# Optimization experiments

Hardware: AMD Instinct MI355X
Metric: run time of the kernel (lower is better)

The kernel has to match this reference:

```python
import jax, jax.numpy as jnp
import numpy as np

# PtConv dims from SegSmall: pl=64 channels, n_centers=16 kernel elements, dim=3
B, N, K = 4, 16384, 16          # batch, points, neighbors
C_IN, C_OUT, KS, DIM = 64, 64, 16, 3


def setup_inputs() -> dict:
    key = jax.random.key(0)
    ks = jax.random.split(key, 10)
    features = jax.random.normal(ks[0], (B, N, C_IN), dtype=jnp.float32)
    input_pts = jax.random.uniform(ks[1], (B, N, DIM), dtype=jnp.float32)
    output_pts = input_pts  # same-resolution conv: queries == input points
    indices = jax.random.randint(ks[2], (B, N, K), 0, N)  # precomputed KNN indices
    # weight init as in PtConv
    bound = float(np.sqrt(3.0) * np.sqrt(2.0 / (C_IN + C_OUT)))
    weight = jax.random.uniform(ks[3], (C_IN, KS, C_OUT), jnp.float32, -bound, bound)
    bias = jnp.zeros((C_OUT,), jnp.float32)
    centers = jax.random.uniform(ks[4], (DIM, KS), jnp.float32, -1.0, 1.0)
    # position-MLP params: Linear(dim*KS -> 2*KS), Linear(2*KS -> KS), Linear(KS -> KS)
    def lin(k, fan_in, fan_out):
        lim = 1.0 / np.sqrt(fan_in)
        kw, kb = jax.random.split(k)
        W = jax.random.uniform(kw, (fan_in, fan_out), jnp.float32, -lim, lim)
        b = jax.random.uniform(kb, (fan_out,), jnp.float32, -lim, lim)
        return W, b
    w1, b1 = lin(ks[5], DIM * KS, 2 * KS)
    w2, b2 = lin(ks[6], 2 * KS, KS)
    w3, b3 = lin(ks[7], KS, KS)
    return {"features": features, "input_pts": input_pts, "output_pts": output_pts,
            "weight": weight, "bias": bias, "centers": centers,
            "w1": w1, "b1": b1, "w2": w2, "b2": b2, "w3": w3, "b3": b3,
            "indices": indices}


def reference(features, input_pts, output_pts, weight, bias, centers,
              w1, b1, w2, b2, w3, b3, indices):
    # per-batch gather of neighbor features and coordinates
    gather = jax.vmap(lambda a, idx: a[idx])
    feat_g = gather(features, indices)          # [B, M, K, C_in]
    pts_g = gather(input_pts, indices)          # [B, M, K, 3]
    pts = pts_g - output_pts[:, :, None, :]      # nn_center=True
    # distances to kernel centers: [B,M,K,3,1] - [3,KS] -> [B,M,K,3,KS] -> [B,M,K,3*KS]
    d = (pts[..., None] - centers).reshape(pts.shape[0], pts.shape[1], pts.shape[2], -1)
    d = jax.nn.relu(d @ w1 + b1)
    d = jax.nn.relu(d @ w2 + b2)
    d = jax.nn.relu(d @ w3 + b3)                 # [B, M, K, KS]
    # weighted neighbor aggregation: bmm(features^T, dists)
    agg = jnp.einsum('bmkc,bmkj->bmcj', feat_g, d)   # [B, M, C_in, KS]
    out = jnp.einsum('bmcj,cjo->bmo', agg, weight)   # flatten (C_in,KS) matches weight.view(-1,out)
    out = out / feat_g.shape[2]                      # divide by K (fs[2])
    out = out + bias
    return out
```

## Files before the change

kernel.cpp:

```cpp
#include <hip/hip_runtime.h>

#define NPTS 16384
#define KN   16
#define CIN  64
#define COUT 64
#define KSIZ 16
#define PTS  16

typedef _Float16 h4v    __attribute__((ext_vector_type(4)));
typedef _Float16 h8v    __attribute__((ext_vector_type(8)));
typedef __fp16   fp16x2 __attribute__((ext_vector_type(2)));
typedef float    f32x4  __attribute__((ext_vector_type(4)));

union H2U { fp16x2 h; unsigned u; };
union H4U { h4v v; fp16x2 p[2]; };
union H8U { h8v v; uint4 u4; };

__global__ void prep_kernel(const float* __restrict__ weight,
                            const float* __restrict__ w1,
                            const float* __restrict__ b1,
                            const float* __restrict__ centers,
                            unsigned* __restrict__ wsp,
                            uint4* __restrict__ wf) {
    const int b = blockIdx.x;
    const int tid = threadIdx.x;
    if (b == 128) {
        __shared__ float tmp[4][32];
        if (tid < 32) {
            int n = tid;
            float s0 = 0.f, s1 = 0.f, s2 = 0.f, bf = b1[n];
            for (int s = 0; s < KSIZ; ++s) {
                float a0 = w1[(0*KSIZ + s)*32 + n];
                float a1 = w1[(1*KSIZ + s)*32 + n];
                float a2 = w1[(2*KSIZ + s)*32 + n];
                s0 += a0; s1 += a1; s2 += a2;
                bf -= centers[0*KSIZ+s]*a0 + centers[1*KSIZ+s]*a1 + centers[2*KSIZ+s]*a2;
            }
            tmp[0][n] = s0; tmp[1][n] = s1; tmp[2][n] = s2; tmp[3][n] = bf;
        }
        __syncthreads();
        if (tid < 64) {
            const int row = tid >> 4, q = tid & 15;
            union { _Float16 h[2]; unsigned u; } pk;
            pk.h[0] = (_Float16)tmp[row][2*q];
            pk.h[1] = (_Float16)tmp[row][2*q+1];
            wsp[row*16 + q] = pk.u;
        }
        return;
    }
    const int kk = b >> 2, nt = b & 3;
    const int l  = tid, li = l & 15, g = l >> 4;
    unsigned short u[8];
    #pragma unroll
    for (int e = 0; e < 8; ++e) {
        int s = kk*32 + g*8 + e;
        int j = s >> 6;
        int c = s & 63;
        union { _Float16 h; unsigned short s16; } cv;
        cv.h = (_Float16)(weight[(c*16 + j)*64 + nt*16 + li] * 0.0625f);
        u[e] = cv.s16;
    }
    uint4 v;
    v.x = u[0] | ((unsigned)u[1] << 16);
    v.y = u[2] | ((unsigned)u[3] << 16);
    v.z = u[4] | ((unsigned)u[5] << 16);
    v.w = u[6] | ((unsigned)u[7] << 16);
    wf[(kk*4 + nt)*64 + l] = v;
}

__global__ __launch_bounds__(256, 4)
void ptconv_kernel(const float* __restrict__ features,
                   const float* __restrict__ input_pts,
                   const float* __restrict__ output_pts,
                   const float* __restrict__ bias,
                   const float* __restrict__ w2,
                   const float* __restrict__ b2,
                   const float* __restrict__ w3,
                   const float* __restrict__ b3,
                   const int*   __restrict__ indices,
                   const unsigned* __restrict__ folded,
                   const uint4* __restrict__ wf,
                   float* __restrict__ out) {
    __shared__ __align__(16) char smem[34048];
    char* s_agg = smem;
    int*  s_idx = (int*)(smem + 33024);

    const int t    = threadIdx.x;
    const int l    = t & 63;
    const int wave = t >> 6;
    const int li   = l & 15;
    const int g    = l >> 4;
    const int m0   = blockIdx.x * PTS;
    const int bbk  = m0 >> 14;

    const int p1 = t >> 4, k1 = t & 15;
    const int nn = (m0 + p1) & (NPTS-1);
    const int idxv = indices[(bbk*NPTS + nn)*KN + k1];
    s_idx[p1*16 + k1] = idxv;
    const float* ip = input_pts  + (size_t)(bbk*NPTS + idxv)*3;
    const float* op = output_pts + (size_t)(bbk*NPTS + nn)*3;
    const float r0 = ip[0]-op[0], r1 = ip[1]-op[1], r2 = ip[2]-op[2];

    h8v w2f; h4v w3f;
    #pragma unroll
    for (int e = 0; e < 8; ++e) w2f[e] = (_Float16)w2[(8*g+e)*16 + li];
    #pragma unroll
    for (int e = 0; e < 4; ++e) w3f[e] = (_Float16)w3[(4*g+e)*16 + li];
    const f32x4 b2v4  = *(const f32x4*)(b2 + 4*g);
    const float b3v   = b3[li];
    const float biasO = bias[wave*16 + li];

    {
        const __fp16 r0h = (__fp16)r0, r1h = (__fp16)r1, r2h = (__fp16)r2;
        fp16x2 r0p = {r0h, r0h}, r1p = {r1h, r1h}, r2p = {r2h, r2h};
        const fp16x2 zz = {(__fp16)0.f, (__fp16)0.f};
        unsigned o16[16];
        #pragma unroll
        for (int q = 0; q < 16; ++q) {
            H2U a, u0, u1, u2;
            a.u  = folded[48+q];
            u0.u = folded[q];
            u1.u = folded[16+q];
            u2.u = folded[32+q];
            fp16x2 acc = r0p*u0.h + a.h;
            acc = r1p*u1.h + acc;
            acc = r2p*u2.h + acc;
            acc = __builtin_elementwise_max(acc, zz);
            H2U o; o.h = acc; o16[q] = o.u;
        }
        uint4* dst = (uint4*)(smem + wave*8256 + l*80);
        dst[0] = make_uint4(o16[0],  o16[1],  o16[2],  o16[3]);
        dst[1] = make_uint4(o16[4],  o16[5],  o16[6],  o16[7]);
        dst[2] = make_uint4(o16[8],  o16[9],  o16[10], o16[11]);
        dst[3] = make_uint4(o16[12], o16[13], o16[14], o16[15]);
    }

    const float* fb = features + (size_t)bbk*NPTS*CIN;
    f32x4 rv[4][4];
    #pragma unroll
    for (int pp = 0; pp < 4; ++pp) {
        const int p2 = wave*4 + pp;
        const int4 id4 = *(const int4*)(s_idx + p2*16 + 4*g);
        rv[pp][0] = *(const f32x4*)(fb + (size_t)id4.x*CIN + 4*li);
        rv[pp][1] = *(const f32x4*)(fb + (size_t)id4.y*CIN + 4*li);
        rv[pp][2] = *(const f32x4*)(fb + (size_t)id4.z*CIN + 4*li);
        rv[pp][3] = *(const f32x4*)(fb + (size_t)id4.w*CIN + 4*li);
    }

    h4v dreg[4];
    #pragma unroll
    for (int pp = 0; pp < 4; ++pp) {
        h8v B2 = *(const h8v*)(smem + wave*8256 + (pp*16 + li)*80 + g*16);
        f32x4 acc2 = b2v4;
        acc2 = __builtin_amdgcn_mfma_f32_16x16x32_f16(w2f, B2, acc2, 0, 0, 0);
        H4U A3;
        A3.p[0] = __builtin_amdgcn_cvt_pkrtz(fmaxf(acc2[0],0.f), fmaxf(acc2[1],0.f));
        A3.p[1] = __builtin_amdgcn_cvt_pkrtz(fmaxf(acc2[2],0.f), fmaxf(acc2[3],0.f));
        f32x4 acc3 = {b3v, b3v, b3v, b3v};
        acc3 = __builtin_amdgcn_mfma_f32_16x16x16f16(A3.v, w3f, acc3, 0, 0, 0);
        H4U Dv;
        Dv.p[0] = __builtin_amdgcn_cvt_pkrtz(fmaxf(acc3[0],0.f), fmaxf(acc3[1],0.f));
        Dv.p[1] = __builtin_amdgcn_cvt_pkrtz(fmaxf(acc3[2],0.f), fmaxf(acc3[3],0.f));
        dreg[pp] = Dv.v;
    }

    #pragma unroll
    for (int pp = 0; pp < 4; ++pp) {
        const int p2 = wave*4 + pp;
        f32x4 pacc[4];
        #pragma unroll
        for (int ct = 0; ct < 4; ++ct) {
            H4U B;
            B.p[0] = __builtin_amdgcn_cvt_pkrtz(rv[pp][0][ct], rv[pp][1][ct]);
            B.p[1] = __builtin_amdgcn_cvt_pkrtz(rv[pp][2][ct], rv[pp][3][ct]);
            f32x4 z = {0.f, 0.f, 0.f, 0.f};
            pacc[ct] = __builtin_amdgcn_mfma_f32_16x16x16f16(dreg[pp], B.v, z, 0, 0, 0);
        }
        #pragma unroll
        for (int r = 0; r < 4; ++r) {
            H2U d01, d23;
            d01.h = __builtin_amdgcn_cvt_pkrtz(pacc[0][r], pacc[1][r]);
            d23.h = __builtin_amdgcn_cvt_pkrtz(pacc[2][r], pacc[3][r]);
            *(uint2*)(s_agg + p2*2064 + (4*g + r)*128 + 8*li) = make_uint2(d01.u, d23.u);
        }
    }

    const uint4* wp = wf + wave*64 + l;
    uint4 wa0 = wp[0*256], wa1 = wp[1*256], wa2 = wp[2*256], wa3 = wp[3*256];
    uint4 wa4 = wp[4*256], wa5 = wp[5*256], wa6 = wp[6*256], wa7 = wp[7*256];

    __syncthreads();

    __builtin_amdgcn_s_setprio(1);
    f32x4 acc = {0.f, 0.f, 0.f, 0.f};
#define AREAD(KK) (*(const h8v*)(s_agg + li*2064 + (KK)*64 + g*16))
#define MF(KK, WREG) { H8U bu_; bu_.u4 = WREG; acc = __builtin_amdgcn_mfma_f32_16x16x32_f16(AREAD(KK), bu_.v, acc, 0, 0, 0); }
    uint4 wb0 = wp[ 8*256], wb1 = wp[ 9*256], wb2 = wp[10*256], wb3 = wp[11*256];
    uint4 wb4 = wp[12*256], wb5 = wp[13*256], wb6 = wp[14*256], wb7 = wp[15*256];
    MF(0, wa0) MF(1, wa1) MF(2, wa2) MF(3, wa3)
    MF(4, wa4) MF(5, wa5) MF(6, wa6) MF(7, wa7)
    uint4 wc0 = wp[16*256], wc1 = wp[17*256], wc2 = wp[18*256], wc3 = wp[19*256];
    uint4 wc4 = wp[20*256], wc5 = wp[21*256], wc6 = wp[22*256], wc7 = wp[23*256];
    MF( 8, wb0) MF( 9, wb1) MF(10, wb2) MF(11, wb3)
    MF(12, wb4) MF(13, wb5) MF(14, wb6) MF(15, wb7)
    uint4 wd0 = wp[24*256], wd1 = wp[25*256], wd2 = wp[26*256], wd3 = wp[27*256];
    uint4 wd4 = wp[28*256], wd5 = wp[29*256], wd6 = wp[30*256], wd7 = wp[31*256];
    MF(16, wc0) MF(17, wc1) MF(18, wc2) MF(19, wc3)
    MF(20, wc4) MF(21, wc5) MF(22, wc6) MF(23, wc7)
    MF(24, wd0) MF(25, wd1) MF(26, wd2) MF(27, wd3)
    MF(28, wd4) MF(29, wd5) MF(30, wd6) MF(31, wd7)
#undef MF
#undef AREAD
    __builtin_amdgcn_s_setprio(0);

    #pragma unroll
    for (int r = 0; r < 4; ++r) {
        const int mr = g*4 + r;
        out[(size_t)(m0 + mr)*COUT + wave*16 + li] = acc[r] + biasO;
    }
}

extern "C" void kernel_launch(void* const* d_in, const int* in_sizes, int n_in,
                              void* d_out, int out_size, void* d_ws, size_t ws_size,
                              hipStream_t stream) {
    const float* features   = (const float*)d_in[0];
    const float* input_pts  = (const float*)d_in[1];
    const float* output_pts = (const float*)d_in[2];
    const float* weight     = (const float*)d_in[3];
    const float* bias       = (const float*)d_in[4];
    const float* centers    = (const float*)d_in[5];
    const float* w1         = (const float*)d_in[6];
    const float* b1         = (const float*)d_in[7];
    const float* w2         = (const float*)d_in[8];
    const float* b2         = (const float*)d_in[9];
    const float* w3         = (const float*)d_in[10];
    const float* b3         = (const float*)d_in[11];
    const int*   indices    = (const int*)d_in[12];
    float* out = (float*)d_out;
    unsigned* wsp = (unsigned*)d_ws;
    uint4* wf = (uint4*)((char*)d_ws + 512);

    prep_kernel<<<129, 64, 0, stream>>>(weight, w1, b1, centers, wsp, wf);

    const int total_pts = 4 * NPTS;
    ptconv_kernel<<<total_pts / PTS, 256, 0, stream>>>(
        features, input_pts, output_pts, bias,
        w2, b2, w3, b3, indices, wsp, wf, out);
}
```

Baseline: 50.15 us.

## Process four point tiles per block with software-pipelined neighbor gathers

Each block now loops over four 16-point tiles instead of one, cutting the grid by four. The next tile's indices, coordinates and feature gathers are prefetched into registers while the current tile's MLP and MFMA stages run, so gather latency overlaps compute. Index staging through shared memory is dropped by reading indices straight from global memory per wave. The cost is higher register pressure from the prefetched tiles, fewer blocks to hide latency across CUs, and an extra barrier per iteration.

```diff
diff --git a/kernel.cpp b/kernel.cpp
--- a/kernel.cpp
+++ b/kernel.cpp
@@ -1,11 +1,12 @@
 #include <hip/hip_runtime.h>
 
-#define NPTS 16384
-#define KN   16
-#define CIN  64
-#define COUT 64
-#define KSIZ 16
-#define PTS  16
+#define NPTS  16384
+#define KN    16
+#define CIN   64
+#define COUT  64
+#define KSIZ  16
+#define PTS   16
+#define ITERS 4
 
 typedef _Float16 h4v    __attribute__((ext_vector_type(4)));
 typedef _Float16 h8v    __attribute__((ext_vector_type(8)));
@@ -81,25 +82,22 @@
                    const unsigned* __restrict__ folded,
                    const uint4* __restrict__ wf,
                    float* __restrict__ out) {
-    __shared__ __align__(16) char smem[34048];
+    __shared__ __align__(16) char smem[33024];
     char* s_agg = smem;
-    int*  s_idx = (int*)(smem + 33024);
 
     const int t    = threadIdx.x;
     const int l    = t & 63;
     const int wave = t >> 6;
     const int li   = l & 15;
     const int g    = l >> 4;
-    const int m0   = blockIdx.x * PTS;
-    const int bbk  = m0 >> 14;
-
-    const int p1 = t >> 4, k1 = t & 15;
-    const int nn = (m0 + p1) & (NPTS-1);
-    const int idxv = indices[(bbk*NPTS + nn)*KN + k1];
-    s_idx[p1*16 + k1] = idxv;
-    const float* ip = input_pts  + (size_t)(bbk*NPTS + idxv)*3;
-    const float* op = output_pts + (size_t)(bbk*NPTS + nn)*3;
-    const float r0 = ip[0]-op[0], r1 = ip[1]-op[1], r2 = ip[2]-op[2];
+    const int base_m0 = blockIdx.x * (PTS*ITERS);
+    const int bbk  = base_m0 >> 14;
+    const int p1   = t >> 4, k1 = t & 15;
+
+    const int*   idxB  = indices    + (size_t)bbk*NPTS*KN;
+    const float* fb    = features   + (size_t)bbk*NPTS*CIN;
+    const float* ptsB  = input_pts  + (size_t)bbk*NPTS*3;
+    const float* optsB = output_pts + (size_t)bbk*NPTS*3;
 
     h8v w2f; h4v w3f;
     #pragma unroll
@@ -109,115 +107,177 @@
     const f32x4 b2v4  = *(const f32x4*)(b2 + 4*g);
     const float b3v   = b3[li];
     const float biasO = bias[wave*16 + li];
-
-    {
-        const __fp16 r0h = (__fp16)r0, r1h = (__fp16)r1, r2h = (__fp16)r2;
-        fp16x2 r0p = {r0h, r0h}, r1p = {r1h, r1h}, r2p = {r2h, r2h};
-        const fp16x2 zz = {(__fp16)0.f, (__fp16)0.f};
-        unsigned o16[16];
-        #pragma unroll
-        for (int q = 0; q < 16; ++q) {
-            H2U a, u0, u1, u2;
-            a.u  = folded[48+q];
-            u0.u = folded[q];
-            u1.u = folded[16+q];
-            u2.u = folded[32+q];
-            fp16x2 acc = r0p*u0.h + a.h;
-            acc = r1p*u1.h + acc;
-            acc = r2p*u2.h + acc;
-            acc = __builtin_elementwise_max(acc, zz);
-            H2U o; o.h = acc; o16[q] = o.u;
-        }
-        uint4* dst = (uint4*)(smem + wave*8256 + l*80);
-        dst[0] = make_uint4(o16[0],  o16[1],  o16[2],  o16[3]);
-        dst[1] = make_uint4(o16[4],  o16[5],  o16[6],  o16[7]);
-        dst[2] = make_uint4(o16[8],  o16[9],  o16[10], o16[11]);
-        dst[3] = make_uint4(o16[12], o16[13], o16[14], o16[15]);
-    }
-
-    const float* fb = features + (size_t)bbk*NPTS*CIN;
-    f32x4 rv[4][4];
-    #pragma unroll
-    for (int pp = 0; pp < 4; ++pp) {
-        const int p2 = wave*4 + pp;
-        const int4 id4 = *(const int4*)(s_idx + p2*16 + 4*g);
-        rv[pp][0] = *(const f32x4*)(fb + (size_t)id4.x*CIN + 4*li);
-        rv[pp][1] = *(const f32x4*)(fb + (size_t)id4.y*CIN + 4*li);
-        rv[pp][2] = *(const f32x4*)(fb + (size_t)id4.z*CIN + 4*li);
-        rv[pp][3] = *(const f32x4*)(fb + (size_t)id4.w*CIN + 4*li);
-    }
-
-    h4v dreg[4];
-    #pragma unroll
-    for (int pp = 0; pp < 4; ++pp) {
-        h8v B2 = *(const h8v*)(smem + wave*8256 + (pp*16 + li)*80 + g*16);
-        f32x4 acc2 = b2v4;
-        acc2 = __builtin_amdgcn_mfma_f32_16x16x32_f16(w2f, B2, acc2, 0, 0, 0);
-        H4U A3;
-        A3.p[0] = __builtin_amdgcn_cvt_pkrtz(fmaxf(acc2[0],0.f), fmaxf(acc2[1],0.f));
-        A3.p[1] = __builtin_amdgcn_cvt_pkrtz(fmaxf(acc2[2],0.f), fmaxf(acc2[3],0.f));
-        f32x4 acc3 = {b3v, b3v, b3v, b3v};
-        acc3 = __builtin_amdgcn_mfma_f32_16x16x16f16(A3.v, w3f, acc3, 0, 0, 0);
-        H4U Dv;
-        Dv.p[0] = __builtin_amdgcn_cvt_pkrtz(fmaxf(acc3[0],0.f), fmaxf(acc3[1],0.f));
-        Dv.p[1] = __builtin_amdgcn_cvt_pkrtz(fmaxf(acc3[2],0.f), fmaxf(acc3[3],0.f));
-        dreg[pp] = Dv.v;
-    }
-
-    #pragma unroll
-    for (int pp = 0; pp < 4; ++pp) {
-        const int p2 = wave*4 + pp;
-        f32x4 pacc[4];
-        #pragma unroll
-        for (int ct = 0; ct < 4; ++ct) {
-            H4U B;
-            B.p[0] = __builtin_amdgcn_cvt_pkrtz(rv[pp][0][ct], rv[pp][1][ct]);
-            B.p[1] = __builtin_amdgcn_cvt_pkrtz(rv[pp][2][ct], rv[pp][3][ct]);
-            f32x4 z = {0.f, 0.f, 0.f, 0.f};
-            pacc[ct] = __builtin_amdgcn_mfma_f32_16x16x16f16(dreg[pp], B.v, z, 0, 0, 0);
-        }
+    const uint4* wp   = wf + wave*64 + l;
+
+    const int nn0 = (base_m0 + p1) & (NPTS-1);
+    const int idxv0 = idxB[nn0*KN + k1];
+    float cop0 = optsB[nn0*3+0], cop1 = optsB[nn0*3+1], cop2 = optsB[nn0*3+2];
+    int4 ia0 = *(const int4*)(idxB + ((base_m0 + wave*4+0)&(NPTS-1))*KN + 4*g);
+    int4 ia1 = *(const int4*)(idxB + ((base_m0 + wave*4+1)&(NPTS-1))*KN + 4*g);
+    int4 ia2 = *(const int4*)(idxB + ((base_m0 + wave*4+2)&(NPTS-1))*KN + 4*g);
+    int4 ia3 = *(const int4*)(idxB + ((base_m0 + wave*4+3)&(NPTS-1))*KN + 4*g);
+    float cip0 = ptsB[(size_t)idxv0*3+0], cip1 = ptsB[(size_t)idxv0*3+1], cip2 = ptsB[(size_t)idxv0*3+2];
+    f32x4 rv00, rv01, rv02, rv03, rv10, rv11, rv12, rv13;
+    f32x4 rv20, rv21, rv22, rv23, rv30, rv31, rv32, rv33;
+#define GATH(DST0,DST1,DST2,DST3, ID) \
+    DST0 = *(const f32x4*)(fb + (size_t)(ID).x*CIN + 4*li); \
+    DST1 = *(const f32x4*)(fb + (size_t)(ID).y*CIN + 4*li); \
+    DST2 = *(const f32x4*)(fb + (size_t)(ID).z*CIN + 4*li); \
+    DST3 = *(const f32x4*)(fb + (size_t)(ID).w*CIN + 4*li);
+    GATH(rv00,rv01,rv02,rv03, ia0)
+    GATH(rv10,rv11,rv12,rv13, ia1)
+    GATH(rv20,rv21,rv22,rv23, ia2)
+    GATH(rv30,rv31,rv32,rv33, ia3)
+
+    #pragma unroll 1
+    for (int it = 0; it < ITERS; ++it) {
+        const int m0i = base_m0 + it*PTS;
+        const bool pf = (it + 1 < ITERS);
+        const int m0n = m0i + PTS;
+
+        int idxvN = 0;
+        float opN0 = 0.f, opN1 = 0.f, opN2 = 0.f;
+        int4 inx0, inx1, inx2, inx3;
+        if (pf) {
+            const int nnN = (m0n + p1) & (NPTS-1);
+            idxvN = idxB[nnN*KN + k1];
+            opN0 = optsB[nnN*3+0]; opN1 = optsB[nnN*3+1]; opN2 = optsB[nnN*3+2];
+            inx0 = *(const int4*)(idxB + ((m0n + wave*4+0)&(NPTS-1))*KN + 4*g);
+            inx1 = *(const int4*)(idxB + ((m0n + wave*4+1)&(NPTS-1))*KN + 4*g);
+            inx2 = *(const int4*)(idxB + ((m0n + wave*4+2)&(NPTS-1))*KN + 4*g);
+            inx3 = *(const int4*)(idxB + ((m0n + wave*4+3)&(NPTS-1))*KN + 4*g);
+        }
+
+        {
+            const float r0 = cip0-cop0, r1 = cip1-cop1, r2 = cip2-cop2;
+            const __fp16 r0h = (__fp16)r0, r1h = (__fp16)r1, r2h = (__fp16)r2;
+            fp16x2 r0p = {r0h, r0h}, r1p = {r1h, r1h}, r2p = {r2h, r2h};
+            const fp16x2 zz = {(__fp16)0.f, (__fp16)0.f};
+            unsigned o16[16];
+            #pragma unroll
+            for (int q = 0; q < 16; ++q) {
+                H2U a, u0, u1, u2;
+                a.u  = folded[48+q];
+                u0.u = folded[q];
+                u1.u = folded[16+q];
+                u2.u = folded[32+q];
+                fp16x2 acc = r0p*u0.h + a.h;
+                acc = r1p*u1.h + acc;
+                acc = r2p*u2.h + acc;
+                acc = __builtin_elementwise_max(acc, zz);
+                H2U o; o.h = acc; o16[q] = o.u;
+            }
+            uint4* dst = (uint4*)(smem + wave*8256 + l*80);
+            dst[0] = make_uint4(o16[0],  o16[1],  o16[2],  o16[3]);
+            dst[1] = make_uint4(o16[4],  o16[5],  o16[6],  o16[7]);
+            dst[2] = make_uint4(o16[8],  o16[9],  o16[10], o16[11]);
+            dst[3] = make_uint4(o16[12], o16[13], o16[14], o16[15]);
+        }
+
+        h4v dreg0, dreg1, dreg2, dreg3;
+#define L23(PP, DREG) { \
+        h8v B2 = *(const h8v*)(smem + wave*8256 + ((PP)*16 + li)*80 + g*16); \
+        f32x4 a2 = b2v4; \
+        a2 = __builtin_amdgcn_mfma_f32_16x16x32_f16(w2f, B2, a2, 0, 0, 0); \
+        H4U A3; \
+        A3.p[0] = __builtin_amdgcn_cvt_pkrtz(fmaxf(a2[0],0.f), fmaxf(a2[1],0.f)); \
+        A3.p[1] = __builtin_amdgcn_cvt_pkrtz(fmaxf(a2[2],0.f), fmaxf(a2[3],0.f)); \
+        f32x4 a3 = {b3v, b3v, b3v, b3v}; \
+        a3 = __builtin_amdgcn_mfma_f32_16x16x16f16(A3.v, w3f, a3, 0, 0, 0); \
+        H4U Dv; \
+        Dv.p[0] = __builtin_amdgcn_cvt_pkrtz(fmaxf(a3[0],0.f), fmaxf(a3[1],0.f)); \
+        Dv.p[1] = __builtin_amdgcn_cvt_pkrtz(fmaxf(a3[2],0.f), fmaxf(a3[3],0.f)); \
+        DREG = Dv.v; }
+        L23(0, dreg0) L23(1, dreg1) L23(2, dreg2) L23(3, dreg3)
+
+#define PHASE2(PP, DREG, R0,R1,R2,R3) { \
+        f32x4 z = {0.f,0.f,0.f,0.f}; \
+        H4U B0c, B1c, B2c, B3c; \
+        B0c.p[0] = __builtin_amdgcn_cvt_pkrtz(R0[0], R1[0]); \
+        B0c.p[1] = __builtin_amdgcn_cvt_pkrtz(R2[0], R3[0]); \
+        B1c.p[0] = __builtin_amdgcn_cvt_pkrtz(R0[1], R1[1]); \
+        B1c.p[1] = __builtin_amdgcn_cvt_pkrtz(R2[1], R3[1]); \
+        B2c.p[0] = __builtin_amdgcn_cvt_pkrtz(R0[2], R1[2]); \
+        B2c.p[1] = __builtin_amdgcn_cvt_pkrtz(R2[2], R3[2]); \
+        B3c.p[0] = __builtin_amdgcn_cvt_pkrtz(R0[3], R1[3]); \
+        B3c.p[1] = __builtin_amdgcn_cvt_pkrtz(R2[3], R3[3]); \
+        f32x4 p0 = __builtin_amdgcn_mfma_f32_16x16x16f16(DREG, B0c.v, z, 0, 0, 0); \
+        f32x4 p1 = __builtin_amdgcn_mfma_f32_16x16x16f16(DREG, B1c.v, z, 0, 0, 0); \
+        f32x4 p2 = __builtin_amdgcn_mfma_f32_16x16x16f16(DREG, B2c.v, z, 0, 0, 0); \
+        f32x4 p3 = __builtin_amdgcn_mfma_f32_16x16x16f16(DREG, B3c.v, z, 0, 0, 0); \
+        char* ab = s_agg + (wave*4 + (PP))*2064 + 8*li; \
+        _Pragma("unroll") \
+        for (int r = 0; r < 4; ++r) { \
+            H2U d01, d23; \
+            d01.h = __builtin_amdgcn_cvt_pkrtz(p0[r], p1[r]); \
+            d23.h = __builtin_amdgcn_cvt_pkrtz(p2[r], p3[r]); \
+            *(uint2*)(ab + (4*g + r)*128) = make_uint2(d01.u, d23.u); \
+        } }
+        PHASE2(0, dreg0, rv00,rv01,rv02,rv03)
+        PHASE2(1, dreg1, rv10,rv11,rv12,rv13)
+
+        float ipN0 = 0.f, ipN1 = 0.f, ipN2 = 0.f;
+        if (pf) {
+            GATH(rv00,rv01,rv02,rv03, inx0)
+            GATH(rv10,rv11,rv12,rv13, inx1)
+            ipN0 = ptsB[(size_t)idxvN*3+0];
+            ipN1 = ptsB[(size_t)idxvN*3+1];
+            ipN2 = ptsB[(size_t)idxvN*3+2];
+        }
+
+        PHASE2(2, dreg2, rv20,rv21,rv22,rv23)
+        PHASE2(3, dreg3, rv30,rv31,rv32,rv33)
+
+        uint4 wa0 = wp[0*256], wa1 = wp[1*256], wa2 = wp[2*256], wa3 = wp[3*256];
+        uint4 wa4 = wp[4*256], wa5 = wp[5*256], wa6 = wp[6*256], wa7 = wp[7*256];
+
+        asm volatile("s_waitcnt lgkmcnt(0)" ::: "memory");
+        __builtin_amdgcn_s_barrier();
+        asm volatile("" ::: "memory");
+
+        __builtin_amdgcn_s_setprio(1);
+        f32x4 acc = {0.f, 0.f, 0.f, 0.f};
+#define AREAD(KK) (*(const h8v*)(s_agg + li*2064 + (KK)*64 + g*16))
+#define MF(KK, WREG) { H8U bu_; bu_.u4 = WREG; acc = __builtin_amdgcn_mfma_f32_16x16x32_f16(AREAD(KK), bu_.v, acc, 0, 0, 0); }
+        uint4 wb0 = wp[ 8*256], wb1 = wp[ 9*256], wb2 = wp[10*256], wb3 = wp[11*256];
+        uint4 wb4 = wp[12*256], wb5 = wp[13*256], wb6 = wp[14*256], wb7 = wp[15*256];
+        MF(0, wa0) MF(1, wa1) MF(2, wa2) MF(3, wa3)
+        MF(4, wa4) MF(5, wa5) MF(6, wa6) MF(7, wa7)
+        uint4 wc0 = wp[16*256], wc1 = wp[17*256], wc2 = wp[18*256], wc3 = wp[19*256];
+        uint4 wc4 = wp[20*256], wc5 = wp[21*256], wc6 = wp[22*256], wc7 = wp[23*256];
+        MF( 8, wb0) MF( 9, wb1) MF(10, wb2) MF(11, wb3)
+        MF(12, wb4) MF(13, wb5) MF(14, wb6) MF(15, wb7)
+        uint4 wd0 = wp[24*256], wd1 = wp[25*256], wd2 = wp[26*256], wd3 = wp[27*256];
+        uint4 wd4 = wp[28*256], wd5 = wp[29*256], wd6 = wp[30*256], wd7 = wp[31*256];
+        MF(16, wc0) MF(17, wc1) MF(18, wc2) MF(19, wc3)
+        MF(20, wc4) MF(21, wc5) MF(22, wc6) MF(23, wc7)
+        MF(24, wd0) MF(25, wd1) MF(26, wd2) MF(27, wd3)
+        MF(28, wd4) MF(29, wd5) MF(30, wd6) MF(31, wd7)
+#undef MF
+#undef AREAD
+        __builtin_amdgcn_s_setprio(0);
+
         #pragma unroll
         for (int r = 0; r < 4; ++r) {
-            H2U d01, d23;
-            d01.h = __builtin_amdgcn_cvt_pkrtz(pacc[0][r], pacc[1][r]);
-            d23.h = __builtin_amdgcn_cvt_pkrtz(pacc[2][r], pacc[3][r]);
-            *(uint2*)(s_agg + p2*2064 + (4*g + r)*128 + 8*li) = make_uint2(d01.u, d23.u);
+            const int mr = g*4 + r;
+            out[(size_t)(m0i + mr)*COUT + wave*16 + li] = acc[r] + biasO;
+        }
+
+        asm volatile("" ::: "memory");
+        __builtin_amdgcn_s_barrier();
+        asm volatile("" ::: "memory");
+
+        if (pf) {
+            GATH(rv20,rv21,rv22,rv23, inx2)
+            GATH(rv30,rv31,rv32,rv33, inx3)
+            asm volatile("" ::: "memory");
+            cip0 = ipN0; cip1 = ipN1; cip2 = ipN2;
+            cop0 = opN0; cop1 = opN1; cop2 = opN2;
         }
     }
-
-    const uint4* wp = wf + wave*64 + l;
-    uint4 wa0 = wp[0*256], wa1 = wp[1*256], wa2 = wp[2*256], wa3 = wp[3*256];
-    uint4 wa4 = wp[4*256], wa5 = wp[5*256], wa6 = wp[6*256], wa7 = wp[7*256];
-
-    __syncthreads();
-
-    __builtin_amdgcn_s_setprio(1);
-    f32x4 acc = {0.f, 0.f, 0.f, 0.f};
-#define AREAD(KK) (*(const h8v*)(s_agg + li*2064 + (KK)*64 + g*16))
-#define MF(KK, WREG) { H8U bu_; bu_.u4 = WREG; acc = __builtin_amdgcn_mfma_f32_16x16x32_f16(AREAD(KK), bu_.v, acc, 0, 0, 0); }
-    uint4 wb0 = wp[ 8*256], wb1 = wp[ 9*256], wb2 = wp[10*256], wb3 = wp[11*256];
-    uint4 wb4 = wp[12*256], wb5 = wp[13*256], wb6 = wp[14*256], wb7 = wp[15*256];
-    MF(0, wa0) MF(1, wa1) MF(2, wa2) MF(3, wa3)
-    MF(4, wa4) MF(5, wa5) MF(6, wa6) MF(7, wa7)
-    uint4 wc0 = wp[16*256], wc1 = wp[17*256], wc2 = wp[18*256], wc3 = wp[19*256];
-    uint4 wc4 = wp[20*256], wc5 = wp[21*256], wc6 = wp[22*256], wc7 = wp[23*256];
-    MF( 8, wb0) MF( 9, wb1) MF(10, wb2) MF(11, wb3)
-    MF(12, wb4) MF(13, wb5) MF(14, wb6) MF(15, wb7)
-    uint4 wd0 = wp[24*256], wd1 = wp[25*256], wd2 = wp[26*256], wd3 = wp[27*256];
-    uint4 wd4 = wp[28*256], wd5 = wp[29*256], wd6 = wp[30*256], wd7 = wp[31*256];
-    MF(16, wc0) MF(17, wc1) MF(18, wc2) MF(19, wc3)
-    MF(20, wc4) MF(21, wc5) MF(22, wc6) MF(23, wc7)
-    MF(24, wd0) MF(25, wd1) MF(26, wd2) MF(27, wd3)
-    MF(28, wd4) MF(29, wd5) MF(30, wd6) MF(31, wd7)
-#undef MF
-#undef AREAD
-    __builtin_amdgcn_s_setprio(0);
-
-    #pragma unroll
-    for (int r = 0; r < 4; ++r) {
-        const int mr = g*4 + r;
-        out[(size_t)(m0 + mr)*COUT + wave*16 + li] = acc[r] + biasO;
-    }
+#undef GATH
+#undef L23
+#undef PHASE2
 }
 
 extern "C" void kernel_launch(void* const* d_in, const int* in_sizes, int n_in,
@@ -243,7 +303,7 @@
     prep_kernel<<<129, 64, 0, stream>>>(weight, w1, b1, centers, wsp, wf);
 
     const int total_pts = 4 * NPTS;
-    ptconv_kernel<<<total_pts / PTS, 256, 0, stream>>>(
+    ptconv_kernel<<<total_pts / (PTS*ITERS), 256, 0, stream>>>(
         features, input_pts, output_pts, bias,
         w2, b2, w3, b3, indices, wsp, wf, out);
 }
```

Result: slower. 164.6 us (+228.2%).

## Pre-convert features to fp16 in workspace and gather half-width rows

Applied to the files above, without the earlier changes.

The prep kernel now also converts the full feature tensor to fp16 in the workspace, so the main kernel gathers 8-byte neighbor rows instead of 16-byte fp32 rows. Neighbor indices are read directly from global memory instead of being staged through LDS, and the LDS aggregate buffer uses an XOR swizzle in place of padding. The final GEMM loop uses four independent accumulators with rolling weight prefetch, and occupancy is raised to five blocks per CU. The cost is an extra full pass over the features (8 MB written) inside the timed launch, plus a fallback path for when the workspace is too small.

```diff
diff --git a/kernel.cpp b/kernel.cpp
--- a/kernel.cpp
+++ b/kernel.cpp
@@ -13,21 +13,47 @@
 typedef float    f32x4  __attribute__((ext_vector_type(4)));
 
 union H2U { fp16x2 h; unsigned u; };
-union H4U { h4v v; fp16x2 p[2]; };
+union H4U { h4v v; fp16x2 p[2]; uint2 u2; };
 union H8U { h8v v; uint4 u4; };
+
+#define WS_WF_OFF   512
+#define WS_F16_OFF  131584
+#define WS_NEEDED   (131584ull + 8388608ull)
 
 __global__ void prep_kernel(const float* __restrict__ weight,
                             const float* __restrict__ w1,
                             const float* __restrict__ b1,
                             const float* __restrict__ centers,
+                            const float* __restrict__ features,
                             unsigned* __restrict__ wsp,
-                            uint4* __restrict__ wf) {
+                            uint4* __restrict__ wf,
+                            uint4* __restrict__ fb16) {
     const int b = blockIdx.x;
-    const int tid = threadIdx.x;
-    if (b == 128) {
+    const int t = threadIdx.x;
+    if (b < 32) {
+        const int bp = b*4 + (t>>6);
+        const int kk = bp >> 2, nt = bp & 3;
+        const int l = t & 63, li = l & 15, g = l >> 4;
+        unsigned short u[8];
+        #pragma unroll
+        for (int e = 0; e < 8; ++e) {
+            int s = kk*32 + g*8 + e;
+            int j = s >> 6;
+            int c = s & 63;
+            union { _Float16 h; unsigned short s16; } cv;
+            cv.h = (_Float16)(weight[(c*16 + j)*64 + nt*16 + li] * 0.0625f);
+            u[e] = cv.s16;
+        }
+        uint4 v;
+        v.x = u[0] | ((unsigned)u[1] << 16);
+        v.y = u[2] | ((unsigned)u[3] << 16);
+        v.z = u[4] | ((unsigned)u[5] << 16);
+        v.w = u[6] | ((unsigned)u[7] << 16);
+        wf[(kk*4 + nt)*64 + l] = v;
+    } else if (b == 32) {
         __shared__ float tmp[4][32];
-        if (tid < 32) {
-            int n = tid;
+        if (t < 32) {
+            int n = t;
             float s0 = 0.f, s1 = 0.f, s2 = 0.f, bf = b1[n];
             for (int s = 0; s < KSIZ; ++s) {
                 float a0 = w1[(0*KSIZ + s)*32 + n];
@@ -39,36 +65,28 @@
             tmp[0][n] = s0; tmp[1][n] = s1; tmp[2][n] = s2; tmp[3][n] = bf;
         }
         __syncthreads();
-        if (tid < 64) {
-            const int row = tid >> 4, q = tid & 15;
+        if (t < 64) {
+            const int row = t >> 4, q = t & 15;
             union { _Float16 h[2]; unsigned u; } pk;
             pk.h[0] = (_Float16)tmp[row][2*q];
             pk.h[1] = (_Float16)tmp[row][2*q+1];
             wsp[row*16 + q] = pk.u;
         }
-        return;
-    }
-    const int kk = b >> 2, nt = b & 3;
-    const int l  = tid, li = l & 15, g = l >> 4;
-    unsigned short u[8];
-    #pragma unroll
-    for (int e = 0; e < 8; ++e) {
-        int s = kk*32 + g*8 + e;
-        int j = s >> 6;
-        int c = s & 63;
-        union { _Float16 h; unsigned short s16; } cv;
-        cv.h = (_Float16)(weight[(c*16 + j)*64 + nt*16 + li] * 0.0625f);
-        u[e] = cv.s16;
-    }
-    uint4 v;
-    v.x = u[0] | ((unsigned)u[1] << 16);
-    v.y = u[2] | ((unsigned)u[3] << 16);
-    v.z = u[4] | ((unsigned)u[5] << 16);
-    v.w = u[6] | ((unsigned)u[7] << 16);
-    wf[(kk*4 + nt)*64 + l] = v;
+    } else {
+        const size_t e0 = ((size_t)(b - 33)*256 + t) * 8;
+        const float4 f0 = *(const float4*)(features + e0);
+        const float4 f1 = *(const float4*)(features + e0 + 4);
+        union { _Float16 h[8]; uint4 v; } o;
+        o.h[0] = (_Float16)f0.x; o.h[1] = (_Float16)f0.y;
+        o.h[2] = (_Float16)f0.z; o.h[3] = (_Float16)f0.w;
+        o.h[4] = (_Float16)f1.x; o.h[5] = (_Float16)f1.y;
+        o.h[6] = (_Float16)f1.z; o.h[7] = (_Float16)f1.w;
+        fb16[e0 >> 3] = o.v;
+    }
 }
 
-__global__ __launch_bounds__(256, 4)
+template<int FM>
+__global__ __launch_bounds__(256, 5)
 void ptconv_kernel(const float* __restrict__ features,
                    const float* __restrict__ input_pts,
                    const float* __restrict__ output_pts,
@@ -80,10 +98,10 @@
                    const int*   __restrict__ indices,
                    const unsigned* __restrict__ folded,
                    const uint4* __restrict__ wf,
+                   const uint2* __restrict__ fb16,
                    float* __restrict__ out) {
-    __shared__ __align__(16) char smem[34048];
+    __shared__ __align__(16) char smem[32768];
     char* s_agg = smem;
-    int*  s_idx = (int*)(smem + 33024);
 
     const int t    = threadIdx.x;
     const int l    = t & 63;
@@ -92,14 +110,49 @@
     const int g    = l >> 4;
     const int m0   = blockIdx.x * PTS;
     const int bbk  = m0 >> 14;
+    const int mloc = m0 & (NPTS-1);
+
+    const int*   idxB  = indices    + (size_t)bbk*NPTS*KN;
+    const float* ptsB  = input_pts  + (size_t)bbk*NPTS*3;
+    const float* optsB = output_pts + (size_t)bbk*NPTS*3;
+    const float* fb    = features + (size_t)bbk*NPTS*CIN;
+    const uint2* fb16B = fb16 + (size_t)bbk*NPTS*(CIN/4);
 
     const int p1 = t >> 4, k1 = t & 15;
-    const int nn = (m0 + p1) & (NPTS-1);
-    const int idxv = indices[(bbk*NPTS + nn)*KN + k1];
-    s_idx[p1*16 + k1] = idxv;
-    const float* ip = input_pts  + (size_t)(bbk*NPTS + idxv)*3;
-    const float* op = output_pts + (size_t)(bbk*NPTS + nn)*3;
-    const float r0 = ip[0]-op[0], r1 = ip[1]-op[1], r2 = ip[2]-op[2];
+    const int nn = mloc + p1;
+    const int idxv = idxB[nn*KN + k1];
+    const float cop0 = optsB[nn*3+0], cop1 = optsB[nn*3+1], cop2 = optsB[nn*3+2];
+    const float cip0 = ptsB[(size_t)idxv*3+0];
+    const float cip1 = ptsB[(size_t)idxv*3+1];
+    const float cip2 = ptsB[(size_t)idxv*3+2];
+
+    const int4 idA = *(const int4*)(idxB + (mloc + wave*4+0)*KN + 4*g);
+    const int4 idB = *(const int4*)(idxB + (mloc + wave*4+1)*KN + 4*g);
+    const int4 idC = *(const int4*)(idxB + (mloc + wave*4+2)*KN + 4*g);
+    const int4 idD = *(const int4*)(idxB + (mloc + wave*4+3)*KN + 4*g);
+
+    H4U gA0, gA1, gA2, gA3, gB0, gB1, gB2, gB3;
+    H4U gC0, gC1, gC2, gC3, gD0, gD1, gD2, gD3;
+    f32x4 fA0, fA1, fA2, fA3, fB0, fB1, fB2, fB3;
+    if constexpr (FM == 1) {
+        gA0.u2 = fb16B[(size_t)idA.x*16 + li]; gA1.u2 = fb16B[(size_t)idA.y*16 + li];
+        gA2.u2 = fb16B[(size_t)idA.z*16 + li]; gA3.u2 = fb16B[(size_t)idA.w*16 + li];
+        gB0.u2 = fb16B[(size_t)idB.x*16 + li]; gB1.u2 = fb16B[(size_t)idB.y*16 + li];
+        gB2.u2 = fb16B[(size_t)idB.z*16 + li]; gB3.u2 = fb16B[(size_t)idB.w*16 + li];
+        gC0.u2 = fb16B[(size_t)idC.x*16 + li]; gC1.u2 = fb16B[(size_t)idC.y*16 + li];
+        gC2.u2 = fb16B[(size_t)idC.z*16 + li]; gC3.u2 = fb16B[(size_t)idC.w*16 + li];
+        gD0.u2 = fb16B[(size_t)idD.x*16 + li]; gD1.u2 = fb16B[(size_t)idD.y*16 + li];
+        gD2.u2 = fb16B[(size_t)idD.z*16 + li]; gD3.u2 = fb16B[(size_t)idD.w*16 + li];
+    } else {
+        fA0 = *(const f32x4*)(fb + (size_t)idA.x*CIN + 4*li);
+        fA1 = *(const f32x4*)(fb + (size_t)idA.y*CIN + 4*li);
+        fA2 = *(const f32x4*)(fb + (size_t)idA.z*CIN + 4*li);
+        fA3 = *(const f32x4*)(fb + (size_t)idA.w*CIN + 4*li);
+        fB0 = *(const f32x4*)(fb + (size_t)idB.x*CIN + 4*li);
+        fB1 = *(const f32x4*)(fb + (size_t)idB.y*CIN + 4*li);
+        fB2 = *(const f32x4*)(fb + (size_t)idB.z*CIN + 4*li);
+        fB3 = *(const f32x4*)(fb + (size_t)idB.w*CIN + 4*li);
+    }
 
     h8v w2f; h4v w3f;
     #pragma unroll
@@ -109,110 +162,146 @@
     const f32x4 b2v4  = *(const f32x4*)(b2 + 4*g);
     const float b3v   = b3[li];
     const float biasO = bias[wave*16 + li];
+    const uint4* wp   = wf + wave*64 + l;
 
     {
-        const __fp16 r0h = (__fp16)r0, r1h = (__fp16)r1, r2h = (__fp16)r2;
+        const __fp16 r0h = (__fp16)(cip0-cop0);
+        const __fp16 r1h = (__fp16)(cip1-cop1);
+        const __fp16 r2h = (__fp16)(cip2-cop2);
         fp16x2 r0p = {r0h, r0h}, r1p = {r1h, r1h}, r2p = {r2h, r2h};
         const fp16x2 zz = {(__fp16)0.f, (__fp16)0.f};
-        unsigned o16[16];
+        uint4* dst = (uint4*)(smem + wave*8192 + l*80);
+        unsigned o8[8];
         #pragma unroll
-        for (int q = 0; q < 16; ++q) {
-            H2U a, u0, u1, u2;
-            a.u  = folded[48+q];
-            u0.u = folded[q];
-            u1.u = folded[16+q];
-            u2.u = folded[32+q];
-            fp16x2 acc = r0p*u0.h + a.h;
-            acc = r1p*u1.h + acc;
-            acc = r2p*u2.h + acc;
-            acc = __builtin_elementwise_max(acc, zz);
-            H2U o; o.h = acc; o16[q] = o.u;
+        for (int half = 0; half < 2; ++half) {
+            #pragma unroll
+            for (int qq = 0; qq < 8; ++qq) {
+                const int q = half*8 + qq;
+                H2U a, u0, u1, u2;
+                a.u  = folded[48+q];
+                u0.u = folded[q];
+                u1.u = folded[16+q];
+                u2.u = folded[32+q];
+                fp16x2 acc = r0p*u0.h + a.h;
+                acc = r1p*u1.h + acc;
+                acc = r2p*u2.h + acc;
+                acc = __builtin_elementwise_max(acc, zz);
+                H2U o; o.h = acc; o8[qq] = o.u;
+            }
+            dst[half*2+0] = make_uint4(o8[0], o8[1], o8[2], o8[3]);
+            dst[half*2+1] = make_uint4(o8[4], o8[5], o8[6], o8[7]);
         }
-        uint4* dst = (uint4*)(smem + wave*8256 + l*80);
-        dst[0] = make_uint4(o16[0],  o16[1],  o16[2],  o16[3]);
-        dst[1] = make_uint4(o16[4],  o16[5],  o16[6],  o16[7]);
-        dst[2] = make_uint4(o16[8],  o16[9],  o16[10], o16[11]);
-        dst[3] = make_uint4(o16[12], o16[13], o16[14], o16[15]);
-    }
-
-    const float* fb = features + (size_t)bbk*NPTS*CIN;
-    f32x4 rv[4][4];
-    #pragma unroll
-    for (int pp = 0; pp < 4; ++pp) {
-        const int p2 = wave*4 + pp;
-        const int4 id4 = *(const int4*)(s_idx + p2*16 + 4*g);
-        rv[pp][0] = *(const f32x4*)(fb + (size_t)id4.x*CIN + 4*li);
-        rv[pp][1] = *(const f32x4*)(fb + (size_t)id4.y*CIN + 4*li);
-        rv[pp][2] = *(const f32x4*)(fb + (size_t)id4.z*CIN + 4*li);
-        rv[pp][3] = *(const f32x4*)(fb + (size_t)id4.w*CIN + 4*li);
-    }
-
-    h4v dreg[4];
-    #pragma unroll
-    for (int pp = 0; pp < 4; ++pp) {
-        h8v B2 = *(const h8v*)(smem + wave*8256 + (pp*16 + li)*80 + g*16);
-        f32x4 acc2 = b2v4;
-        acc2 = __builtin_amdgcn_mfma_f32_16x16x32_f16(w2f, B2, acc2, 0, 0, 0);
-        H4U A3;
-        A3.p[0] = __builtin_amdgcn_cvt_pkrtz(fmaxf(acc2[0],0.f), fmaxf(acc2[1],0.f));
-        A3.p[1] = __builtin_amdgcn_cvt_pkrtz(fmaxf(acc2[2],0.f), fmaxf(acc2[3],0.f));
-        f32x4 acc3 = {b3v, b3v, b3v, b3v};
-        acc3 = __builtin_amdgcn_mfma_f32_16x16x16f16(A3.v, w3f, acc3, 0, 0, 0);
-        H4U Dv;
-        Dv.p[0] = __builtin_amdgcn_cvt_pkrtz(fmaxf(acc3[0],0.f), fmaxf(acc3[1],0.f));
-        Dv.p[1] = __builtin_amdgcn_cvt_pkrtz(fmaxf(acc3[2],0.f), fmaxf(acc3[3],0.f));
-        dreg[pp] = Dv.v;
-    }
-
-    #pragma unroll
-    for (int pp = 0; pp < 4; ++pp) {
-        const int p2 = wave*4 + pp;
-        f32x4 pacc[4];
-        #pragma unroll
-        for (int ct = 0; ct < 4; ++ct) {
-            H4U B;
-            B.p[0] = __builtin_amdgcn_cvt_pkrtz(rv[pp][0][ct], rv[pp][1][ct]);
-            B.p[1] = __builtin_amdgcn_cvt_pkrtz(rv[pp][2][ct], rv[pp][3][ct]);
-            f32x4 z = {0.f, 0.f, 0.f, 0.f};
-            pacc[ct] = __builtin_amdgcn_mfma_f32_16x16x16f16(dreg[pp], B.v, z, 0, 0, 0);
-        }
-        #pragma unroll
-        for (int r = 0; r < 4; ++r) {
-            H2U d01, d23;
-            d01.h = __builtin_amdgcn_cvt_pkrtz(pacc[0][r], pacc[1][r]);
-            d23.h = __builtin_amdgcn_cvt_pkrtz(pacc[2][r], pacc[3][r]);
-            *(uint2*)(s_agg + p2*2064 + (4*g + r)*128 + 8*li) = make_uint2(d01.u, d23.u);
-        }
-    }
-
-    const uint4* wp = wf + wave*64 + l;
-    uint4 wa0 = wp[0*256], wa1 = wp[1*256], wa2 = wp[2*256], wa3 = wp[3*256];
-    uint4 wa4 = wp[4*256], wa5 = wp[5*256], wa6 = wp[6*256], wa7 = wp[7*256];
-
-    __syncthreads();
+    }
+
+    h4v dreg0, dreg1, dreg2, dreg3;
+#define L23(PP, DREG) { \
+    h8v B2 = *(const h8v*)(smem + wave*8192 + ((PP)*16 + li)*80 + g*16); \
+    f32x4 a2 = b2v4; \
+    a2 = __builtin_amdgcn_mfma_f32_16x16x32_f16(w2f, B2, a2, 0, 0, 0); \
+    H4U A3; \
+    A3.p[0] = __builtin_amdgcn_cvt_pkrtz(fmaxf(a2[0],0.f), fmaxf(a2[1],0.f)); \
+    A3.p[1] = __builtin_amdgcn_cvt_pkrtz(fmaxf(a2[2],0.f), fmaxf(a2[3],0.f)); \
+    f32x4 a3 = {b3v, b3v, b3v, b3v}; \
+    a3 = __builtin_amdgcn_mfma_f32_16x16x16f16(A3.v, w3f, a3, 0, 0, 0); \
+    H4U Dv; \
+    Dv.p[0] = __builtin_amdgcn_cvt_pkrtz(fmaxf(a3[0],0.f), fmaxf(a3[1],0.f)); \
+    Dv.p[1] = __builtin_amdgcn_cvt_pkrtz(fmaxf(a3[2],0.f), fmaxf(a3[3],0.f)); \
+    DREG = Dv.v; }
+    L23(0, dreg0) L23(1, dreg1) L23(2, dreg2) L23(3, dreg3)
+#undef L23
+
+#define P2STORE(PP, E0,E1,E2,E3) { \
+    const int pix_ = wave*4 + (PP); \
+    const unsigned swz_ = (unsigned)((pix_ & 7) << 4); \
+    char* ab_ = s_agg + pix_*2048; \
+    _Pragma("unroll") \
+    for (int r = 0; r < 4; ++r) { \
+        H2U d01, d23; \
+        d01.h = __builtin_amdgcn_cvt_pkrtz(E0[r], E1[r]); \
+        d23.h = __builtin_amdgcn_cvt_pkrtz(E2[r], E3[r]); \
+        *(uint2*)(ab_ + ((unsigned)((4*g + r)*128 + 8*li) ^ swz_)) = \
+            make_uint2(d01.u, d23.u); \
+    } }
+
+    if constexpr (FM == 1) {
+#define P2F16(PP, R0,R1,R2,R3) { \
+        f32x4 z = {0.f,0.f,0.f,0.f}; \
+        f32x4 e0_, e1_, e2_, e3_; \
+        { H4U B_; B_.v = (h4v){R0.v[0], R1.v[0], R2.v[0], R3.v[0]}; \
+          e0_ = __builtin_amdgcn_mfma_f32_16x16x16f16(dreg##PP, B_.v, z, 0, 0, 0); } \
+        { H4U B_; B_.v = (h4v){R0.v[1], R1.v[1], R2.v[1], R3.v[1]}; \
+          e1_ = __builtin_amdgcn_mfma_f32_16x16x16f16(dreg##PP, B_.v, z, 0, 0, 0); } \
+        { H4U B_; B_.v = (h4v){R0.v[2], R1.v[2], R2.v[2], R3.v[2]}; \
+          e2_ = __builtin_amdgcn_mfma_f32_16x16x16f16(dreg##PP, B_.v, z, 0, 0, 0); } \
+        { H4U B_; B_.v = (h4v){R0.v[3], R1.v[3], R2.v[3], R3.v[3]}; \
+          e3_ = __builtin_amdgcn_mfma_f32_16x16x16f16(dreg##PP, B_.v, z, 0, 0, 0); } \
+        P2STORE(PP, e0_, e1_, e2_, e3_) }
+        P2F16(0, gA0, gA1, gA2, gA3)
+        P2F16(1, gB0, gB1, gB2, gB3)
+        P2F16(2, gC0, gC1, gC2, gC3)
+        P2F16(3, gD0, gD1, gD2, gD3)
+#undef P2F16
+    } else {
+#define P2F32(PP, R0,R1,R2,R3) { \
+        f32x4 z = {0.f,0.f,0.f,0.f}; \
+        f32x4 e0_, e1_, e2_, e3_; \
+        { H4U B_; B_.p[0] = __builtin_amdgcn_cvt_pkrtz(R0[0], R1[0]); \
+          B_.p[1] = __builtin_amdgcn_cvt_pkrtz(R2[0], R3[0]); \
+          e0_ = __builtin_amdgcn_mfma_f32_16x16x16f16(dreg##PP, B_.v, z, 0, 0, 0); } \
+        { H4U B_; B_.p[0] = __builtin_amdgcn_cvt_pkrtz(R0[1], R1[1]); \
+          B_.p[1] = __builtin_amdgcn_cvt_pkrtz(R2[1], R3[1]); \
+          e1_ = __builtin_amdgcn_mfma_f32_16x16x16f16(dreg##PP, B_.v, z, 0, 0, 0); } \
+        { H4U B_; B_.p[0] = __builtin_amdgcn_cvt_pkrtz(R0[2], R1[2]); \
+          B_.p[1] = __builtin_amdgcn_cvt_pkrtz(R2[2], R3[2]); \
+          e2_ = __builtin_amdgcn_mfma_f32_16x16x16f16(dreg##PP, B_.v, z, 0, 0, 0); } \
+        { H4U B_; B_.p[0] = __builtin_amdgcn_cvt_pkrtz(R0[3], R1[3]); \
+          B_.p[1] = __builtin_amdgcn_cvt_pkrtz(R2[3], R3[3]); \
+          e3_ = __builtin_amdgcn_mfma_f32_16x16x16f16(dreg##PP, B_.v, z, 0, 0, 0); } \
+        P2STORE(PP, e0_, e1_, e2_, e3_) }
+        P2F32(0, fA0, fA1, fA2, fA3)
+        P2F32(1, fB0, fB1, fB2, fB3)
+        fA0 = *(const f32x4*)(fb + (size_t)idC.x*CIN + 4*li);
+        fA1 = *(const f32x4*)(fb + (size_t)idC.y*CIN + 4*li);
+        fA2 = *(const f32x4*)(fb + (size_t)idC.z*CIN + 4*li);
+        fA3 = *(const f32x4*)(fb + (size_t)idC.w*CIN + 4*li);
+        fB0 = *(const f32x4*)(fb + (size_t)idD.x*CIN + 4*li);
+        fB1 = *(const f32x4*)(fb + (size_t)idD.y*CIN + 4*li);
+        fB2 = *(const f32x4*)(fb + (size_t)idD.z*CIN + 4*li);
+        fB3 = *(const f32x4*)(fb + (size_t)idD.w*CIN + 4*li);
+        P2F32(2, fA0, fA1, fA2, fA3)
+        P2F32(3, fB0, fB1, fB2, fB3)
+#undef P2F32
+    }
+#undef P2STORE
+
+    uint4 q0 = wp[0*256], q1 = wp[1*256], q2 = wp[2*256], q3 = wp[3*256];
+    uint4 q4 = wp[4*256], q5 = wp[5*256], q6 = wp[6*256], q7 = wp[7*256];
+
+    asm volatile("s_waitcnt lgkmcnt(0)" ::: "memory");
+    __builtin_amdgcn_s_barrier();
+    asm volatile("" ::: "memory");
 
     __builtin_amdgcn_s_setprio(1);
-    f32x4 acc = {0.f, 0.f, 0.f, 0.f};
-#define AREAD(KK) (*(const h8v*)(s_agg + li*2064 + (KK)*64 + g*16))
-#define MF(KK, WREG) { H8U bu_; bu_.u4 = WREG; acc = __builtin_amdgcn_mfma_f32_16x16x32_f16(AREAD(KK), bu_.v, acc, 0, 0, 0); }
-    uint4 wb0 = wp[ 8*256], wb1 = wp[ 9*256], wb2 = wp[10*256], wb3 = wp[11*256];
-    uint4 wb4 = wp[12*256], wb5 = wp[13*256], wb6 = wp[14*256], wb7 = wp[15*256];
-    MF(0, wa0) MF(1, wa1) MF(2, wa2) MF(3, wa3)
-    MF(4, wa4) MF(5, wa5) MF(6, wa6) MF(7, wa7)
-    uint4 wc0 = wp[16*256], wc1 = wp[17*256], wc2 = wp[18*256], wc3 = wp[19*256];
-    uint4 wc4 = wp[20*256], wc5 = wp[21*256], wc6 = wp[22*256], wc7 = wp[23*256];
-    MF( 8, wb0) MF( 9, wb1) MF(10, wb2) MF(11, wb3)
-    MF(12, wb4) MF(13, wb5) MF(14, wb6) MF(15, wb7)
-    uint4 wd0 = wp[24*256], wd1 = wp[25*256], wd2 = wp[26*256], wd3 = wp[27*256];
-    uint4 wd4 = wp[28*256], wd5 = wp[29*256], wd6 = wp[30*256], wd7 = wp[31*256];
-    MF(16, wc0) MF(17, wc1) MF(18, wc2) MF(19, wc3)
-    MF(20, wc4) MF(21, wc5) MF(22, wc6) MF(23, wc7)
-    MF(24, wd0) MF(25, wd1) MF(26, wd2) MF(27, wd3)
-    MF(28, wd4) MF(29, wd5) MF(30, wd6) MF(31, wd7)
-#undef MF
+    f32x4 a0 = {0.f,0.f,0.f,0.f}, a1 = a0, a2 = a0, a3 = a0;
+    const unsigned swr = (unsigned)((li & 7) << 4);
+#define AREAD(KK) (*(const h8v*)(s_agg + li*2048 + (((KK)*64 + g*16) ^ swr)))
+#define MFS(KK, Q, ACC)  { H8U bu_; bu_.u4 = Q; \
+    ACC = __builtin_amdgcn_mfma_f32_16x16x32_f16(AREAD(KK), bu_.v, ACC, 0, 0, 0); }
+#define MFSL(KK, Q, ACC) MFS(KK, Q, ACC) Q = wp[((KK)+8)*256];
+    MFSL(0, q0, a0) MFSL(1, q1, a1) MFSL(2, q2, a2) MFSL(3, q3, a3)
+    MFSL(4, q4, a0) MFSL(5, q5, a1) MFSL(6, q6, a2) MFSL(7, q7, a3)
+    MFSL(8, q0, a0) MFSL(9, q1, a1) MFSL(10, q2, a2) MFSL(11, q3, a3)
+    MFSL(12, q4, a0) MFSL(13, q5, a1) MFSL(14, q6, a2) MFSL(15, q7, a3)
+    MFSL(16, q0, a0) MFSL(17, q1, a1) MFSL(18, q2, a2) MFSL(19, q3, a3)
+    MFSL(20, q4, a0) MFSL(21, q5, a1) MFSL(22, q6, a2) MFSL(23, q7, a3)
+    MFS(24, q0, a0) MFS(25, q1, a1) MFS(26, q2, a2) MFS(27, q3, a3)
+    MFS(28, q4, a0) MFS(29, q5, a1) MFS(30, q6, a2) MFS(31, q7, a3)
+#undef MFSL
+#undef MFS
 #undef AREAD
     __builtin_amdgcn_s_setprio(0);
 
+    const f32x4 acc = (a0 + a1) + (a2 + a3);
     #pragma unroll
     for (int r = 0; r < 4; ++r) {
         const int mr = g*4 + r;
@@ -238,12 +327,22 @@
     const int*   indices    = (const int*)d_in[12];
     float* out = (float*)d_out;
     unsigned* wsp = (unsigned*)d_ws;
-    uint4* wf = (uint4*)((char*)d_ws + 512);
-
-    prep_kernel<<<129, 64, 0, stream>>>(weight, w1, b1, centers, wsp, wf);
+    uint4* wf   = (uint4*)((char*)d_ws + WS_WF_OFF);
+    uint4* fb16 = (uint4*)((char*)d_ws + WS_F16_OFF);
+
+    const bool f16ok = ws_size >= WS_NEEDED;
+    const int nconv = f16ok ? (4*NPTS*CIN) / (256*8) : 0;
+    prep_kernel<<<33 + nconv, 256, 0, stream>>>(
+        weight, w1, b1, centers, features, wsp, wf, fb16);
 
     const int total_pts = 4 * NPTS;
-    ptconv_kernel<<<total_pts / PTS, 256, 0, stream>>>(
-        features, input_pts, output_pts, bias,
-        w2, b2, w3, b3, indices, wsp, wf, out);
+    if (f16ok) {
+        ptconv_kernel<1><<<total_pts / PTS, 256, 0, stream>>>(
+            features, input_pts, output_pts, bias,
+            w2, b2, w3, b3, indices, wsp, wf, (const uint2*)fb16, out);
+    } else {
+        ptconv_kernel<0><<<total_pts / PTS, 256, 0, stream>>>(
+            features, input_pts, output_pts, bias,
+            w2, b2, w3, b3, indices, wsp, wf, (const uint2*)fb16, out);
+    }
 }
```

Measured after the change: 48.21 us. 1.04x faster.
